# Kernel tuning notes

Measured on AMD Instinct MI355X. Metric: run time of the kernel, lower is better.

The kernel has to match this reference:

```python
import jax, jax.numpy as jnp
import numpy as np

T, L, C = 256, 32, 8
B, D = 16, 512


def _content_matrix(T, L, C):
    # Faithful port of compute_content_matrix: binary indicator (L, L, C, T).
    # Only upper-triangular (i <= j) window pairs are populated.
    Wc = np.zeros((L, L, C, T), dtype=np.float32)
    stride = T // L
    for i in range(L):
        for j in range(i, L):
            window_size = j - i + 1
            window_start = i * stride
            num_frames = window_size * stride
            clip_size = num_frames // C if num_frames > C else 1
            for c in range(min(C, num_frames)):
                clip_start = window_start + c * clip_size
                Wc[i, j, c, clip_start:clip_start + clip_size] = 1.0
    return Wc


def setup_inputs() -> dict:
    key = jax.random.key(0)
    f = jax.random.normal(key, (B, T, D), dtype=jnp.float32)
    Wc = jnp.asarray(_content_matrix(T, L, C))
    return {"f": f, "Wc": Wc}


def reference(f, Wc):
    # fc[b,l,m,c,d] = sum_t Wc[l,m,c,t] * f[b,t,d]  -> clip content features
    fc = jnp.einsum('lmct,btd->blmcd', Wc, f)  # (B, L, L, C, D)
    # fm: sum over clips within each window
    fm = jnp.sum(fc, axis=3)  # (B, L, L, D)
    # NOTE: original torch code overwrites the avg-pooled tensor with a fresh
    # permute of f, so fb is just f transposed (the pooling result is discarded).
    fb = jnp.transpose(f, (0, 2, 1))  # (B, D, T)
    return fc, fm, fb
```

## Files before the change

kernel.cpp:

```cpp
#include <hip/hip_runtime.h>

#define TT 256
#define LL 32
#define CC 8
#define BB 16
#define DD 512
#define D4 (DD / 4)
#define NCHUNK 16
#define CHUNK 16

#define FC_ELEMS ((long)BB * LL * LL * CC * DD)
#define FM_ELEMS ((long)BB * LL * LL * DD)
#define FM_OFF   FC_ELEMS
#define FB_OFF   (FC_ELEMS + FM_ELEMS)

#define CSUM_FLOATS ((long)BB * NCHUNK * DD)
#define S_ROWS      (TT + 1)
#define S_OFF_FLOATS CSUM_FLOATS

__global__ __launch_bounds__(256) void chunk_sum_kernel(
    const float* __restrict__ f, float* __restrict__ csum) {
  int tid = blockIdx.x * blockDim.x + threadIdx.x;
  int d = tid & (DD - 1);
  int chunk = (tid >> 9) & (NCHUNK - 1);
  int b = tid >> 13;
  const float* fp = f + ((long)(b * TT + chunk * CHUNK)) * DD + d;
  float s = 0.f;
#pragma unroll
  for (int i = 0; i < CHUNK; ++i) s += fp[(long)i * DD];
  csum[tid] = s;
}

__global__ __launch_bounds__(256) void scan_kernel(
    const float* __restrict__ f, const float* __restrict__ csum,
    float* __restrict__ S, float* __restrict__ fb) {
  int tid = blockIdx.x * blockDim.x + threadIdx.x;
  int d = tid & (DD - 1);
  int chunk = (tid >> 9) & (NCHUNK - 1);
  int b = tid >> 13;

  const float* cp = csum + (long)b * NCHUNK * DD + d;
  float off = 0.f;
  for (int i = 0; i < chunk; ++i) off += cp[(long)i * DD];

  const float* fp = f + ((long)(b * TT + chunk * CHUNK)) * DD + d;
  float* Sp = S + ((long)b * S_ROWS + chunk * CHUNK) * DD + d;
  if (chunk == 0) Sp[0] = 0.f;

  float vals[CHUNK];
  float acc = off;
#pragma unroll
  for (int i = 0; i < CHUNK; ++i) {
    float x = fp[(long)i * DD];
    vals[i] = x;
    acc += x;
    Sp[(long)(i + 1) * DD] = acc;
  }

  float4* fbp = (float4*)(fb + ((long)(b * DD + d)) * TT + chunk * CHUNK);
#pragma unroll
  for (int i = 0; i < 4; ++i) {
    float4 v;
    v.x = vals[4 * i + 0];
    v.y = vals[4 * i + 1];
    v.z = vals[4 * i + 2];
    v.w = vals[4 * i + 3];
    fbp[i] = v;
  }
}

__global__ __launch_bounds__(128) void fc_fm_kernel(
    const float* __restrict__ S, float* __restrict__ out) {
  int m = blockIdx.x;
  int l = blockIdx.y;
  int b = blockIdx.z;
  int d4 = threadIdx.x;

  float4* outv = (float4*)out;
  long blm = (long)((b * LL + l) * LL + m);
  long fc_base = blm * CC * D4;
  long fm_base = FM_OFF / 4 + blm * D4;

  if (l > m) {
    float4 z = {0.f, 0.f, 0.f, 0.f};
#pragma unroll
    for (int c = 0; c < CC; ++c) outv[fc_base + (long)c * D4 + d4] = z;
    outv[fm_base + d4] = z;
    return;
  }

  int w = m - l + 1;
  const float4* S4 = (const float4*)S;
  long srow = (long)b * S_ROWS;

  float4 s[9];
#pragma unroll
  for (int c = 0; c <= 8; ++c) {
    int p = 8 * l + c * w;
    s[c] = S4[(srow + p) * D4 + d4];
  }

#pragma unroll
  for (int c = 0; c < CC; ++c) {
    float4 v;
    v.x = s[c + 1].x - s[c].x;
    v.y = s[c + 1].y - s[c].y;
    v.z = s[c + 1].z - s[c].z;
    v.w = s[c + 1].w - s[c].w;
    outv[fc_base + (long)c * D4 + d4] = v;
  }
  float4 vm;
  vm.x = s[8].x - s[0].x;
  vm.y = s[8].y - s[0].y;
  vm.z = s[8].z - s[0].z;
  vm.w = s[8].w - s[0].w;
  outv[fm_base + d4] = vm;
}

extern "C" void kernel_launch(void* const* d_in, const int* in_sizes, int n_in,
                              void* d_out, int out_size, void* d_ws, size_t ws_size,
                              hipStream_t stream) {
  const float* f = (const float*)d_in[0];
  float* out = (float*)d_out;

  float* csum = (float*)d_ws;
  float* S = (float*)d_ws + S_OFF_FLOATS;

  float* fb = out + FB_OFF;

  {
    int total = BB * NCHUNK * DD;
    chunk_sum_kernel<<<total / 256, 256, 0, stream>>>(f, csum);
    scan_kernel<<<total / 256, 256, 0, stream>>>(f, csum, S, fb);
  }
  {
    dim3 grid(LL, LL, BB);
    fc_fm_kernel<<<grid, 128, 0, stream>>>(S, out);
  }
}
```

Baseline: 329.6 us.

## Vectorize prefix-sum kernels to float4 and remap fc_fm blocks across XCDs

The chunk-sum and scan kernels now have each thread handle four adjacent d channels using float4 loads and stores, with a 4x4 register transpose for the fb output. This cuts thread count and memory instructions but leaves fewer threads in the small pre-pass. The fc_fm kernel moves to a 1D grid whose block index is permuted so consecutive blocks on the same XCD cover contiguous (b,l,m) regions. That is meant to improve L2 locality of the S reads and the output writes. The fc_fm kernel dominates, since it writes a very large output.

```diff
diff --git a/kernel.cpp b/kernel.cpp
--- a/kernel.cpp
+++ b/kernel.cpp
@@ -18,62 +18,69 @@
 #define S_ROWS      (TT + 1)
 #define S_OFF_FLOATS CSUM_FLOATS
 
+__device__ __forceinline__ float4 f4add(float4 a, float4 b) {
+  return make_float4(a.x + b.x, a.y + b.y, a.z + b.z, a.w + b.w);
+}
+__device__ __forceinline__ float4 f4sub(float4 a, float4 b) {
+  return make_float4(a.x - b.x, a.y - b.y, a.z - b.z, a.w - b.w);
+}
+
 __global__ __launch_bounds__(256) void chunk_sum_kernel(
-    const float* __restrict__ f, float* __restrict__ csum) {
+    const float4* __restrict__ f4, float4* __restrict__ csum4) {
   int tid = blockIdx.x * blockDim.x + threadIdx.x;
-  int d = tid & (DD - 1);
-  int chunk = (tid >> 9) & (NCHUNK - 1);
-  int b = tid >> 13;
-  const float* fp = f + ((long)(b * TT + chunk * CHUNK)) * DD + d;
-  float s = 0.f;
+  int d4 = tid & (D4 - 1);
+  int chunk = (tid >> 7) & (NCHUNK - 1);
+  int b = tid >> 11;
+  const float4* fp = f4 + (long)(b * TT + chunk * CHUNK) * D4 + d4;
+  float4 s = make_float4(0.f, 0.f, 0.f, 0.f);
 #pragma unroll
-  for (int i = 0; i < CHUNK; ++i) s += fp[(long)i * DD];
-  csum[tid] = s;
+  for (int i = 0; i < CHUNK; ++i) s = f4add(s, fp[(long)i * D4]);
+  csum4[tid] = s;
 }
 
 __global__ __launch_bounds__(256) void scan_kernel(
-    const float* __restrict__ f, const float* __restrict__ csum,
-    float* __restrict__ S, float* __restrict__ fb) {
+    const float4* __restrict__ f4, const float4* __restrict__ csum4,
+    float4* __restrict__ S4, float4* __restrict__ fb4) {
   int tid = blockIdx.x * blockDim.x + threadIdx.x;
-  int d = tid & (DD - 1);
-  int chunk = (tid >> 9) & (NCHUNK - 1);
-  int b = tid >> 13;
+  int d4 = tid & (D4 - 1);
+  int chunk = (tid >> 7) & (NCHUNK - 1);
+  int b = tid >> 11;
 
-  const float* cp = csum + (long)b * NCHUNK * DD + d;
-  float off = 0.f;
-  for (int i = 0; i < chunk; ++i) off += cp[(long)i * DD];
+  const float4* cp = csum4 + (long)b * NCHUNK * D4 + d4;
+  float4 acc = make_float4(0.f, 0.f, 0.f, 0.f);
+  for (int i = 0; i < chunk; ++i) acc = f4add(acc, cp[(long)i * D4]);
 
-  const float* fp = f + ((long)(b * TT + chunk * CHUNK)) * DD + d;
-  float* Sp = S + ((long)b * S_ROWS + chunk * CHUNK) * DD + d;
-  if (chunk == 0) Sp[0] = 0.f;
+  const float4* fp = f4 + (long)(b * TT + chunk * CHUNK) * D4 + d4;
+  float4* Sp = S4 + ((long)b * S_ROWS + chunk * CHUNK) * D4 + d4;
+  if (chunk == 0) Sp[0] = make_float4(0.f, 0.f, 0.f, 0.f);
 
-  float vals[CHUNK];
-  float acc = off;
+  float4 vals[CHUNK];
 #pragma unroll
   for (int i = 0; i < CHUNK; ++i) {
-    float x = fp[(long)i * DD];
-    vals[i] = x;
-    acc += x;
-    Sp[(long)(i + 1) * DD] = acc;
+    vals[i] = fp[(long)i * D4];
+    acc = f4add(acc, vals[i]);
+    Sp[(long)(i + 1) * D4] = acc;
   }
 
-  float4* fbp = (float4*)(fb + ((long)(b * DD + d)) * TT + chunk * CHUNK);
+  const float* v = (const float*)vals;
 #pragma unroll
-  for (int i = 0; i < 4; ++i) {
-    float4 v;
-    v.x = vals[4 * i + 0];
-    v.y = vals[4 * i + 1];
-    v.z = vals[4 * i + 2];
-    v.w = vals[4 * i + 3];
-    fbp[i] = v;
+  for (int dd = 0; dd < 4; ++dd) {
+    float4* fbp = fb4 + ((long)(b * DD + 4 * d4 + dd) * TT + chunk * CHUNK) / 4;
+#pragma unroll
+    for (int j = 0; j < 4; ++j) {
+      fbp[j] = make_float4(v[(4 * j + 0) * 4 + dd], v[(4 * j + 1) * 4 + dd],
+                           v[(4 * j + 2) * 4 + dd], v[(4 * j + 3) * 4 + dd]);
+    }
   }
 }
 
 __global__ __launch_bounds__(128) void fc_fm_kernel(
     const float* __restrict__ S, float* __restrict__ out) {
-  int m = blockIdx.x;
-  int l = blockIdx.y;
-  int b = blockIdx.z;
+  int i = blockIdx.x;
+  int vblk = ((i & 7) << 11) | (i >> 3);
+  int b = vblk >> 10;
+  int l = (vblk >> 5) & (LL - 1);
+  int m = vblk & (LL - 1);
   int d4 = threadIdx.x;
 
   float4* outv = (float4*)out;
@@ -82,7 +89,7 @@
   long fm_base = FM_OFF / 4 + blm * D4;
 
   if (l > m) {
-    float4 z = {0.f, 0.f, 0.f, 0.f};
+    float4 z = make_float4(0.f, 0.f, 0.f, 0.f);
 #pragma unroll
     for (int c = 0; c < CC; ++c) outv[fc_base + (long)c * D4 + d4] = z;
     outv[fm_base + d4] = z;
@@ -101,40 +108,27 @@
   }
 
 #pragma unroll
-  for (int c = 0; c < CC; ++c) {
-    float4 v;
-    v.x = s[c + 1].x - s[c].x;
-    v.y = s[c + 1].y - s[c].y;
-    v.z = s[c + 1].z - s[c].z;
-    v.w = s[c + 1].w - s[c].w;
-    outv[fc_base + (long)c * D4 + d4] = v;
-  }
-  float4 vm;
-  vm.x = s[8].x - s[0].x;
-  vm.y = s[8].y - s[0].y;
-  vm.z = s[8].z - s[0].z;
-  vm.w = s[8].w - s[0].w;
-  outv[fm_base + d4] = vm;
+  for (int c = 0; c < CC; ++c)
+    outv[fc_base + (long)c * D4 + d4] = f4sub(s[c + 1], s[c]);
+  outv[fm_base + d4] = f4sub(s[8], s[0]);
 }
 
 extern "C" void kernel_launch(void* const* d_in, const int* in_sizes, int n_in,
                               void* d_out, int out_size, void* d_ws, size_t ws_size,
                               hipStream_t stream) {
-  const float* f = (const float*)d_in[0];
+  const float4* f4 = (const float4*)d_in[0];
   float* out = (float*)d_out;
 
-  float* csum = (float*)d_ws;
-  float* S = (float*)d_ws + S_OFF_FLOATS;
-
-  float* fb = out + FB_OFF;
+  float4* csum4 = (float4*)d_ws;
+  float4* S4 = (float4*)((float*)d_ws + S_OFF_FLOATS);
+  float4* fb4 = (float4*)(out + FB_OFF);
 
   {
-    int total = BB * NCHUNK * DD;
-    chunk_sum_kernel<<<total / 256, 256, 0, stream>>>(f, csum);
-    scan_kernel<<<total / 256, 256, 0, stream>>>(f, csum, S, fb);
+    int total4 = BB * NCHUNK * D4;
+    chunk_sum_kernel<<<total4 / 256, 256, 0, stream>>>(f4, csum4);
+    scan_kernel<<<total4 / 256, 256, 0, stream>>>(f4, csum4, S4, fb4);
   }
   {
-    dim3 grid(LL, LL, BB);
-    fc_fm_kernel<<<grid, 128, 0, stream>>>(S, out);
+    fc_fm_kernel<<<BB * LL * LL, 128, 0, stream>>>((const float*)S4, out);
   }
 }
```

Result: no change. 324.0 us (-1.7%).
